# Kernel tuning notes

Measured on AMD Instinct MI355X. Metric: run time of the kernel, lower is better.

## Reference

```python
import jax, jax.numpy as jnp
import numpy as np

MD = 20          # max_displacement
TEMP = 1e-4      # softmax temperature
B, C, H, W = 4, 64, 112, 112


def setup_inputs() -> dict:
    key = jax.random.key(0)
    k1, k2 = jax.random.split(key)
    in1 = jax.random.normal(k1, (B, C, H, W), dtype=jnp.float32)
    in2 = jax.random.normal(k2, (B, C, H, W), dtype=jnp.float32)
    return {"in1": in1, "in2": in2}


def reference(in1, in2):
    b, c, h, w = in1.shape
    # F.normalize(x, dim=1): x / max(||x||_2, eps)
    def l2n(x):
        return x / jnp.maximum(jnp.linalg.norm(x, axis=1, keepdims=True), 1e-12)
    in1 = l2n(in1)
    in2 = l2n(in2)

    pad = jnp.pad(in2, ((0, 0), (0, 0), (MD, MD), (MD, MD)))

    d = jnp.arange(-MD, MD + 1)
    dx, dy = jnp.meshgrid(d, d, indexing="ij")  # torch.meshgrid default 'ij'
    dx = dx.reshape(-1)  # [K] with K = (2*MD+1)^2
    dy = dy.reshape(-1)

    def sim_one(dxi, dyi):
        # shifted window of padded in2, same spatial size as in1
        sl = jax.lax.dynamic_slice(pad, (0, 0, MD + dxi, MD + dyi), (b, c, h, w))
        return jnp.sum(in1 * sl, axis=1)  # [B,H,W]

    sim = jax.vmap(sim_one)(dx, dy)          # [K,B,H,W]
    sim = jnp.transpose(sim, (1, 0, 2, 3))   # [B,K,H,W] cost volume

    weights = jax.nn.softmax(sim / TEMP, axis=1)  # softmax over displacements
    guide = jnp.stack((dx, dy), axis=-1).astype(jnp.float32)  # [K,2]
    # flow[b,d,h,w] = sum_k weights[b,k,h,w] * guide[k,d]
    flow = jnp.einsum("bkhw,kd->bdhw", weights, guide)
    return flow
```

## Files before the change

kernel.cpp:

```cpp
#include <hip/hip_runtime.h>
#include <math.h>

#define BB 4
#define CC 64
#define HH 112
#define WW 112
#define MD 20
#define KD 41
#define SCALE 10000.0f
#define NPIX (BB*HH*WW)
#define NT 10
#define ROW2 (NT*2*2*64*8)
#define IN2S_BYTES ((size_t)BB*HH*ROW2*2)

typedef _Float16 half8   __attribute__((ext_vector_type(8)));
typedef float    f32x4   __attribute__((ext_vector_type(4)));
typedef unsigned short ushort8 __attribute__((ext_vector_type(8)));

static __device__ __forceinline__ unsigned short f2h_bits(float x) {
    _Float16 h = (_Float16)x;
    return __builtin_bit_cast(unsigned short, h);
}
static __device__ __forceinline__ float h2f(unsigned short s) {
    return (float)__builtin_bit_cast(_Float16, s);
}

__global__ __launch_bounds__(256) void prep_kernel(const float* __restrict__ in1,
                                                   const float* __restrict__ in2,
                                                   unsigned short* __restrict__ in2s,
                                                   float* __restrict__ inv1) {
    __shared__ float sinv2[WW];
    int bid = blockIdx.x;
    int b = bid / HH, h = bid % HH;
    int t = threadIdx.x;

    if (t < WW) {
        float s = 0.f;
        for (int c = 0; c < CC; ++c) {
            float x = in2[((b*CC + c)*HH + h)*WW + t];
            s += x*x;
        }
        sinv2[t] = 1.0f / fmaxf(sqrtf(s), 1e-12f);
    } else if (t >= 128 && t < 128 + WW) {
        int w = t - 128;
        float s = 0.f;
        for (int c = 0; c < CC; ++c) {
            float x = in1[((b*CC + c)*HH + h)*WW + w];
            s += x*x;
        }
        inv1[(b*HH + h)*WW + w] = 1.0f / fmaxf(sqrtf(s), 1e-12f);
    }
    __syncthreads();

    int wave = t >> 6, lane = t & 63;
    int n = lane & 15, q = lane >> 4;
    unsigned short* base = in2s + (size_t)(b*HH + h)*ROW2;
    for (int tsk = wave; tsk < NT*2; tsk += 4) {
        int tau = tsk >> 1, ks = tsk & 1;
        int p = 16*tau + n, col = p - MD;
        ushort8 hb = {0,0,0,0,0,0,0,0}, lb = {0,0,0,0,0,0,0,0};
        if (col >= 0 && col < WW) {
            float iv = sinv2[col];
            #pragma unroll
            for (int j = 0; j < 8; ++j) {
                int c = 32*ks + 8*q + j;
                float x = in2[((b*CC + c)*HH + h)*WW + col] * iv;
                unsigned short xh = f2h_bits(x);
                float r = (x - h2f(xh)) * 4096.0f;
                hb[j] = xh;
                lb[j] = f2h_bits(r);
            }
        }
        *(ushort8*)(base + (size_t)((tau*4 + ks*2 + 0)*64 + lane)*8) = hb;
        *(ushort8*)(base + (size_t)((tau*4 + ks*2 + 1)*64 + lane)*8) = lb;
    }
}

__global__ __launch_bounds__(64, 3) void corr_kernel(const float* __restrict__ in1,
                                                     const unsigned short* __restrict__ in2s,
                                                     const float* __restrict__ inv1,
                                                     float* __restrict__ out) {
    int gid = blockIdx.x;
    int wt  = gid / (BB*HH);
    int rem = gid % (BB*HH);
    int b = rem / HH, h = rem % HH;
    int lane = threadIdx.x;
    int n = lane & 15, q = lane >> 4;
    int m0 = 4*q;

    int wA = wt*16 + n;
    float i1 = inv1[(b*HH + h)*WW + wA];
    half8 aH[2], aL[2];
    #pragma unroll
    for (int ks = 0; ks < 2; ++ks) {
        #pragma unroll
        for (int j = 0; j < 8; ++j) {
            int c = 32*ks + 8*q + j;
            float x = in1[((b*CC + c)*HH + h)*WW + wA] * i1;
            _Float16 xh = (_Float16)x;
            aH[ks][j] = xh;
            aL[ks][j] = (_Float16)((x - (float)xh) * 4096.0f);
        }
    }

    float nm20[4]; bool v0[4], v2[4], v3[4];
    #pragma unroll
    for (int r = 0; r < 4; ++r) {
        int nm = n - (m0 + r);
        nm20[r] = (float)(nm - 20);
        v0[r] = (nm >= 0);
        v2[r] = (nm <= 8);
        v3[r] = (nm <= -8);
    }

    float sm[4], sl[4], ssx[4], ssy[4];
    #pragma unroll
    for (int r = 0; r < 4; ++r) { sm[r] = -3.0f; sl[r] = 0.f; ssx[r] = 0.f; ssy[r] = 0.f; }

    int dlo = max(0, MD - h);
    int dhi = min(KD, HH + MD - h);

    for (int dxi = dlo; dxi < dhi; ++dxi) {
        const unsigned short* rb = in2s + (size_t)(b*HH + (h + dxi - MD))*ROW2;
        f32x4 s[4];
        #pragma unroll
        for (int oi = 0; oi < 4; ++oi) {
            int tau = wt + oi;
            const half8* fp = (const half8*)(rb + (size_t)(tau*4*64 + lane)*8);
            half8 bH0 = fp[0];
            half8 bL0 = fp[64];
            half8 bH1 = fp[128];
            half8 bL1 = fp[192];
            f32x4 a0 = {0.f,0.f,0.f,0.f}, a1 = {0.f,0.f,0.f,0.f};
            a0 = __builtin_amdgcn_mfma_f32_16x16x32_f16(aH[0], bH0, a0, 0, 0, 0);
            a1 = __builtin_amdgcn_mfma_f32_16x16x32_f16(aH[0], bL0, a1, 0, 0, 0);
            a1 = __builtin_amdgcn_mfma_f32_16x16x32_f16(aL[0], bH0, a1, 0, 0, 0);
            a0 = __builtin_amdgcn_mfma_f32_16x16x32_f16(aH[1], bH1, a0, 0, 0, 0);
            a1 = __builtin_amdgcn_mfma_f32_16x16x32_f16(aH[1], bL1, a1, 0, 0, 0);
            a1 = __builtin_amdgcn_mfma_f32_16x16x32_f16(aL[1], bH1, a1, 0, 0, 0);
            s[oi] = a0 + a1 * (1.0f/4096.0f);
        }
        float dxf = (float)(dxi - MD);
        #pragma unroll
        for (int r = 0; r < 4; ++r) {
            float s0v = v0[r] ? s[0][r] : -3.0f;
            float s1v = s[1][r];
            float s2v = v2[r] ? s[2][r] : -3.0f;
            float s3v = v3[r] ? s[3][r] : -3.0f;
            float mn = fmaxf(fmaxf(sm[r], s0v), fmaxf(fmaxf(s1v, s2v), s3v));
            float er = __expf((sm[r] - mn)*SCALE);
            float e0 = __expf((s0v - mn)*SCALE);
            float e1 = __expf((s1v - mn)*SCALE);
            float e2 = __expf((s2v - mn)*SCALE);
            float e3 = __expf((s3v - mn)*SCALE);
            float sum = (e0 + e1) + (e2 + e3);
            float tt  = e1 + 2.f*e2 + 3.f*e3;
            sl[r]  = sl[r]*er + sum;
            ssx[r] = ssx[r]*er + dxf*sum;
            ssy[r] = ssy[r]*er + (16.f*tt + nm20[r]*sum);
            sm[r]  = mn;
        }
    }

    int nlo = dlo, nhi = KD - dhi;
    if (nlo + nhi > 0) {
        float sdx = 0.f;
        for (int d = 0; d < nlo; ++d)  sdx += (float)(d - MD);
        for (int d = dhi; d < KD; ++d) sdx += (float)(d - MD);
        float cnt = (float)((nlo + nhi)*KD);
        #pragma unroll
        for (int r = 0; r < 4; ++r) {
            float mn = fmaxf(sm[r], 0.f);
            float er = __expf((sm[r] - mn)*SCALE);
            float e0 = __expf((0.f - mn)*SCALE);
            sl[r]  = sl[r]*er + cnt*e0;
            ssx[r] = ssx[r]*er + (float)KD*sdx*e0;
            ssy[r] = ssy[r]*er;
            sm[r]  = mn;
        }
    }

    #pragma unroll
    for (int off = 1; off < 16; off <<= 1) {
        #pragma unroll
        for (int r = 0; r < 4; ++r) {
            float m2 = __shfl_xor(sm[r],  off);
            float l2 = __shfl_xor(sl[r],  off);
            float x2 = __shfl_xor(ssx[r], off);
            float y2 = __shfl_xor(ssy[r], off);
            float mn = fmaxf(sm[r], m2);
            float ea = __expf((sm[r] - mn)*SCALE);
            float eb = __expf((m2    - mn)*SCALE);
            sl[r]  = sl[r]*ea  + l2*eb;
            ssx[r] = ssx[r]*ea + x2*eb;
            ssy[r] = ssy[r]*ea + y2*eb;
            sm[r]  = mn;
        }
    }

    if (n == 0) {
        #pragma unroll
        for (int r = 0; r < 4; ++r) {
            int w = wt*16 + m0 + r;
            out[((b*2 + 0)*HH + h)*WW + w] = ssx[r] / sl[r];
            out[((b*2 + 1)*HH + h)*WW + w] = ssy[r] / sl[r];
        }
    }
}

extern "C" void kernel_launch(void* const* d_in, const int* in_sizes, int n_in,
                              void* d_out, int out_size, void* d_ws, size_t ws_size,
                              hipStream_t stream) {
    const float* in1 = (const float*)d_in[0];
    const float* in2 = (const float*)d_in[1];
    float* out = (float*)d_out;
    unsigned short* in2s = (unsigned short*)d_ws;
    float* inv1 = (float*)((char*)d_ws + IN2S_BYTES);

    prep_kernel<<<BB*HH, 256, 0, stream>>>(in1, in2, in2s, inv1);
    corr_kernel<<<7*BB*HH, 64, 0, stream>>>(in1, in2s, inv1, out);
}
```

Baseline: 187.9 us.

## Stage in2 tile in LDS, fuse in1 norm into corr, remap blocks per XCD

The pack kernel now loads each in2 row into a shared-memory tile once and reuses it for both the norm and the split-fp16 packing. It no longer computes the in1 norms; the correlation kernel computes them itself with cross-lane shuffles. The correlation kernel uses 128-thread blocks holding two rows 56 apart, and maps block ids so each XCD works on one batch and half the rows, aiming to improve L2 locality of in2s. It also switches to exp2 with a prescaled constant, loads all B fragments before the MFMAs, and drops the occupancy hint from the launch bounds.

```diff
diff --git a/kernel.cpp b/kernel.cpp
--- a/kernel.cpp
+++ b/kernel.cpp
@@ -1,5 +1,4 @@
 #include <hip/hip_runtime.h>
-#include <math.h>
 
 #define BB 4
 #define CC 64
@@ -7,16 +6,15 @@
 #define WW 112
 #define MD 20
 #define KD 41
-#define SCALE 10000.0f
-#define NPIX (BB*HH*WW)
+#define S2 14426.950408f
 #define NT 10
 #define ROW2 (NT*2*2*64*8)
-#define IN2S_BYTES ((size_t)BB*HH*ROW2*2)
 
 typedef _Float16 half8   __attribute__((ext_vector_type(8)));
 typedef float    f32x4   __attribute__((ext_vector_type(4)));
 typedef unsigned short ushort8 __attribute__((ext_vector_type(8)));
 
+static __device__ __forceinline__ float fmax_f(float a, float b) { return a > b ? a : b; }
 static __device__ __forceinline__ unsigned short f2h_bits(float x) {
     _Float16 h = (_Float16)x;
     return __builtin_bit_cast(unsigned short, h);
@@ -24,51 +22,59 @@
 static __device__ __forceinline__ float h2f(unsigned short s) {
     return (float)__builtin_bit_cast(_Float16, s);
 }
-
-__global__ __launch_bounds__(256) void prep_kernel(const float* __restrict__ in1,
-                                                   const float* __restrict__ in2,
-                                                   unsigned short* __restrict__ in2s,
-                                                   float* __restrict__ inv1) {
-    __shared__ float sinv2[WW];
-    int bid = blockIdx.x;
-    int b = bid / HH, h = bid % HH;
+static __device__ __forceinline__ f32x4 vmax4(f32x4 a, f32x4 b) {
+    f32x4 r;
+    #pragma unroll
+    for (int k = 0; k < 4; ++k) r[k] = a[k] > b[k] ? a[k] : b[k];
+    return r;
+}
+static __device__ __forceinline__ f32x4 vexp4(f32x4 d) {
+    f32x4 r;
+    #pragma unroll
+    for (int k = 0; k < 4; ++k) r[k] = __builtin_amdgcn_exp2f(d[k]);
+    return r;
+}
+static __device__ __forceinline__ f32x4 mfma16(half8 a, half8 b, f32x4 c) {
+    return __builtin_amdgcn_mfma_f32_16x16x32_f16(a, b, c, 0, 0, 0);
+}
+
+__global__ __launch_bounds__(256) void pack_kernel(const float* __restrict__ in2,
+                                                   unsigned short* __restrict__ in2s) {
+    __shared__ float tile[CC][WW + 1];
+    __shared__ float sinv[WW];
+    int b = blockIdx.x / HH, h = blockIdx.x % HH;
     int t = threadIdx.x;
-
+    const float* src = in2 + ((size_t)(b*CC)*HH + h)*WW;
+
+    for (int i = t; i < CC*WW; i += 256) {
+        int c = i / WW, w = i % WW;
+        tile[c][w] = src[(size_t)c*(HH*WW) + w];
+    }
+    __syncthreads();
     if (t < WW) {
         float s = 0.f;
-        for (int c = 0; c < CC; ++c) {
-            float x = in2[((b*CC + c)*HH + h)*WW + t];
-            s += x*x;
-        }
-        sinv2[t] = 1.0f / fmaxf(sqrtf(s), 1e-12f);
-    } else if (t >= 128 && t < 128 + WW) {
-        int w = t - 128;
-        float s = 0.f;
-        for (int c = 0; c < CC; ++c) {
-            float x = in1[((b*CC + c)*HH + h)*WW + w];
-            s += x*x;
-        }
-        inv1[(b*HH + h)*WW + w] = 1.0f / fmaxf(sqrtf(s), 1e-12f);
+        #pragma unroll
+        for (int c = 0; c < CC; ++c) { float x = tile[c][t]; s += x*x; }
+        sinv[t] = 1.0f / fmax_f(__builtin_sqrtf(s), 1e-12f);
     }
     __syncthreads();
 
-    int wave = t >> 6, lane = t & 63;
+    int wv = t >> 6, lane = t & 63;
     int n = lane & 15, q = lane >> 4;
     unsigned short* base = in2s + (size_t)(b*HH + h)*ROW2;
-    for (int tsk = wave; tsk < NT*2; tsk += 4) {
-        int tau = tsk >> 1, ks = tsk & 1;
-        int p = 16*tau + n, col = p - MD;
+    for (int u = wv; u < NT*2; u += 4) {
+        int tau = u >> 1, ks = u & 1;
+        int col = 16*tau + n - MD;
         ushort8 hb = {0,0,0,0,0,0,0,0}, lb = {0,0,0,0,0,0,0,0};
         if (col >= 0 && col < WW) {
-            float iv = sinv2[col];
+            float iv = sinv[col];
             #pragma unroll
             for (int j = 0; j < 8; ++j) {
                 int c = 32*ks + 8*q + j;
-                float x = in2[((b*CC + c)*HH + h)*WW + col] * iv;
+                float x = tile[c][col] * iv;
                 unsigned short xh = f2h_bits(x);
-                float r = (x - h2f(xh)) * 4096.0f;
                 hb[j] = xh;
-                lb[j] = f2h_bits(r);
+                lb[j] = f2h_bits((x - h2f(xh)) * 4096.0f);
             }
         }
         *(ushort8*)(base + (size_t)((tau*4 + ks*2 + 0)*64 + lane)*8) = hb;
@@ -76,134 +82,149 @@
     }
 }
 
-__global__ __launch_bounds__(64, 3) void corr_kernel(const float* __restrict__ in1,
-                                                     const unsigned short* __restrict__ in2s,
-                                                     const float* __restrict__ inv1,
-                                                     float* __restrict__ out) {
+__global__ __launch_bounds__(128) void corr_kernel(const float* __restrict__ in1,
+                                                   const unsigned short* __restrict__ in2s,
+                                                   float* __restrict__ out) {
     int gid = blockIdx.x;
-    int wt  = gid / (BB*HH);
-    int rem = gid % (BB*HH);
-    int b = rem / HH, h = rem % HH;
-    int lane = threadIdx.x;
+    int xcd = gid & 7;
+    int s   = gid >> 3;
+    int b   = xcd >> 1;
+    int p   = (xcd & 1)*28 + (s % 28);
+    int wt  = s / 28;
+    int wv  = threadIdx.x >> 6;
+    int h   = p + 56*wv;
+    int lane = threadIdx.x & 63;
     int n = lane & 15, q = lane >> 4;
     int m0 = 4*q;
-
     int wA = wt*16 + n;
-    float i1 = inv1[(b*HH + h)*WW + wA];
+
+    const float* a_src = in1 + ((size_t)(b*CC)*HH + h)*WW + wA;
+    float x[16];
+    float ss = 0.f;
+    #pragma unroll
+    for (int ks = 0; ks < 2; ++ks)
+        #pragma unroll
+        for (int j = 0; j < 8; ++j) {
+            float v = a_src[(size_t)(32*ks + 8*q + j)*(HH*WW)];
+            x[ks*8 + j] = v;
+            ss += v*v;
+        }
+    ss += __shfl_xor(ss, 16);
+    ss += __shfl_xor(ss, 32);
+    float i1 = 1.0f / fmax_f(__builtin_sqrtf(ss), 1e-12f);
     half8 aH[2], aL[2];
     #pragma unroll
-    for (int ks = 0; ks < 2; ++ks) {
+    for (int ks = 0; ks < 2; ++ks)
         #pragma unroll
         for (int j = 0; j < 8; ++j) {
-            int c = 32*ks + 8*q + j;
-            float x = in1[((b*CC + c)*HH + h)*WW + wA] * i1;
-            _Float16 xh = (_Float16)x;
-            aH[ks][j] = xh;
-            aL[ks][j] = (_Float16)((x - (float)xh) * 4096.0f);
-        }
-    }
-
-    float nm20[4]; bool v0[4], v2[4], v3[4];
+            float v = x[ks*8 + j] * i1;
+            _Float16 vh = (_Float16)v;
+            aH[ks][j] = vh;
+            aL[ks][j] = (_Float16)((v - (float)vh) * 4096.0f);
+        }
+
+    f32x4 NM20; bool v0b[4], v2b[4], v3b[4];
     #pragma unroll
     for (int r = 0; r < 4; ++r) {
         int nm = n - (m0 + r);
-        nm20[r] = (float)(nm - 20);
-        v0[r] = (nm >= 0);
-        v2[r] = (nm <= 8);
-        v3[r] = (nm <= -8);
-    }
-
-    float sm[4], sl[4], ssx[4], ssy[4];
-    #pragma unroll
-    for (int r = 0; r < 4; ++r) { sm[r] = -3.0f; sl[r] = 0.f; ssx[r] = 0.f; ssy[r] = 0.f; }
-
-    int dlo = max(0, MD - h);
-    int dhi = min(KD, HH + MD - h);
+        NM20[r] = (float)(nm - 20);
+        v0b[r] = (nm >= 0);
+        v2b[r] = (nm <= 8);
+        v3b[r] = (nm <= -8);
+    }
+
+    f32x4 SM = {-4.f,-4.f,-4.f,-4.f}, SL = {0.f,0.f,0.f,0.f};
+    f32x4 SSX = {0.f,0.f,0.f,0.f}, SSY = {0.f,0.f,0.f,0.f};
+
+    int dlo = MD - h > 0 ? MD - h : 0;
+    int dhi = (HH + MD - h) < KD ? (HH + MD - h) : KD;
 
     for (int dxi = dlo; dxi < dhi; ++dxi) {
         const unsigned short* rb = in2s + (size_t)(b*HH + (h + dxi - MD))*ROW2;
-        f32x4 s[4];
+        half8 bf[4][4];
         #pragma unroll
         for (int oi = 0; oi < 4; ++oi) {
-            int tau = wt + oi;
-            const half8* fp = (const half8*)(rb + (size_t)(tau*4*64 + lane)*8);
-            half8 bH0 = fp[0];
-            half8 bL0 = fp[64];
-            half8 bH1 = fp[128];
-            half8 bL1 = fp[192];
+            const half8* fp = (const half8*)(rb + (size_t)((wt + oi)*4*64 + lane)*8);
+            bf[oi][0] = fp[0];
+            bf[oi][1] = fp[64];
+            bf[oi][2] = fp[128];
+            bf[oi][3] = fp[192];
+        }
+        f32x4 sv[4];
+        #pragma unroll
+        for (int oi = 0; oi < 4; ++oi) {
             f32x4 a0 = {0.f,0.f,0.f,0.f}, a1 = {0.f,0.f,0.f,0.f};
-            a0 = __builtin_amdgcn_mfma_f32_16x16x32_f16(aH[0], bH0, a0, 0, 0, 0);
-            a1 = __builtin_amdgcn_mfma_f32_16x16x32_f16(aH[0], bL0, a1, 0, 0, 0);
-            a1 = __builtin_amdgcn_mfma_f32_16x16x32_f16(aL[0], bH0, a1, 0, 0, 0);
-            a0 = __builtin_amdgcn_mfma_f32_16x16x32_f16(aH[1], bH1, a0, 0, 0, 0);
-            a1 = __builtin_amdgcn_mfma_f32_16x16x32_f16(aH[1], bL1, a1, 0, 0, 0);
-            a1 = __builtin_amdgcn_mfma_f32_16x16x32_f16(aL[1], bH1, a1, 0, 0, 0);
-            s[oi] = a0 + a1 * (1.0f/4096.0f);
-        }
+            a0 = mfma16(aH[0], bf[oi][0], a0);
+            a1 = mfma16(aH[0], bf[oi][1], a1);
+            a1 = mfma16(aL[0], bf[oi][0], a1);
+            a0 = mfma16(aH[1], bf[oi][2], a0);
+            a1 = mfma16(aH[1], bf[oi][3], a1);
+            a1 = mfma16(aL[1], bf[oi][2], a1);
+            sv[oi] = a0 + a1 * (1.0f/4096.0f);
+        }
+        f32x4 V0, V1 = sv[1], V2, V3;
+        #pragma unroll
+        for (int r = 0; r < 4; ++r) {
+            V0[r] = v0b[r] ? sv[0][r] : -4.0f;
+            V2[r] = v2b[r] ? sv[2][r] : -4.0f;
+            V3[r] = v3b[r] ? sv[3][r] : -4.0f;
+        }
+        f32x4 MN = vmax4(vmax4(SM, V0), vmax4(V1, vmax4(V2, V3)));
+        f32x4 ER = vexp4((SM - MN) * S2);
+        f32x4 E0 = vexp4((V0 - MN) * S2);
+        f32x4 E1 = vexp4((V1 - MN) * S2);
+        f32x4 E2 = vexp4((V2 - MN) * S2);
+        f32x4 E3 = vexp4((V3 - MN) * S2);
+        f32x4 SUM = (E0 + E1) + (E2 + E3);
+        f32x4 TT  = E1 + E2*2.0f + E3*3.0f;
         float dxf = (float)(dxi - MD);
-        #pragma unroll
-        for (int r = 0; r < 4; ++r) {
-            float s0v = v0[r] ? s[0][r] : -3.0f;
-            float s1v = s[1][r];
-            float s2v = v2[r] ? s[2][r] : -3.0f;
-            float s3v = v3[r] ? s[3][r] : -3.0f;
-            float mn = fmaxf(fmaxf(sm[r], s0v), fmaxf(fmaxf(s1v, s2v), s3v));
-            float er = __expf((sm[r] - mn)*SCALE);
-            float e0 = __expf((s0v - mn)*SCALE);
-            float e1 = __expf((s1v - mn)*SCALE);
-            float e2 = __expf((s2v - mn)*SCALE);
-            float e3 = __expf((s3v - mn)*SCALE);
-            float sum = (e0 + e1) + (e2 + e3);
-            float tt  = e1 + 2.f*e2 + 3.f*e3;
-            sl[r]  = sl[r]*er + sum;
-            ssx[r] = ssx[r]*er + dxf*sum;
-            ssy[r] = ssy[r]*er + (16.f*tt + nm20[r]*sum);
-            sm[r]  = mn;
-        }
-    }
-
-    int nlo = dlo, nhi = KD - dhi;
-    if (nlo + nhi > 0) {
+        SL  = SL *ER + SUM;
+        SSX = SSX*ER + SUM*dxf;
+        SSY = SSY*ER + (TT*16.0f + NM20*SUM);
+        SM  = MN;
+    }
+
+    int miss = dlo + (KD - dhi);
+    if (miss > 0) {
         float sdx = 0.f;
-        for (int d = 0; d < nlo; ++d)  sdx += (float)(d - MD);
+        for (int d = 0; d < dlo; ++d)  sdx += (float)(d - MD);
         for (int d = dhi; d < KD; ++d) sdx += (float)(d - MD);
-        float cnt = (float)((nlo + nhi)*KD);
-        #pragma unroll
-        for (int r = 0; r < 4; ++r) {
-            float mn = fmaxf(sm[r], 0.f);
-            float er = __expf((sm[r] - mn)*SCALE);
-            float e0 = __expf((0.f - mn)*SCALE);
-            sl[r]  = sl[r]*er + cnt*e0;
-            ssx[r] = ssx[r]*er + (float)KD*sdx*e0;
-            ssy[r] = ssy[r]*er;
-            sm[r]  = mn;
-        }
+        float cnt = (float)miss * (float)KD;
+        f32x4 Z = {0.f,0.f,0.f,0.f};
+        f32x4 MN = vmax4(SM, Z);
+        f32x4 ER = vexp4((SM - MN) * S2);
+        f32x4 E0 = vexp4((Z  - MN) * S2);
+        SL  = SL *ER + E0*cnt;
+        SSX = SSX*ER + E0*((float)KD*sdx);
+        SSY = SSY*ER;
+        SM  = MN;
     }
 
     #pragma unroll
     for (int off = 1; off < 16; off <<= 1) {
-        #pragma unroll
-        for (int r = 0; r < 4; ++r) {
-            float m2 = __shfl_xor(sm[r],  off);
-            float l2 = __shfl_xor(sl[r],  off);
-            float x2 = __shfl_xor(ssx[r], off);
-            float y2 = __shfl_xor(ssy[r], off);
-            float mn = fmaxf(sm[r], m2);
-            float ea = __expf((sm[r] - mn)*SCALE);
-            float eb = __expf((m2    - mn)*SCALE);
-            sl[r]  = sl[r]*ea  + l2*eb;
-            ssx[r] = ssx[r]*ea + x2*eb;
-            ssy[r] = ssy[r]*ea + y2*eb;
-            sm[r]  = mn;
-        }
+        f32x4 M2, L2, X2, Y2;
+        #pragma unroll
+        for (int k = 0; k < 4; ++k) {
+            M2[k] = __shfl_xor(SM[k],  off);
+            L2[k] = __shfl_xor(SL[k],  off);
+            X2[k] = __shfl_xor(SSX[k], off);
+            Y2[k] = __shfl_xor(SSY[k], off);
+        }
+        f32x4 MN = vmax4(SM, M2);
+        f32x4 EA = vexp4((SM - MN) * S2);
+        f32x4 EB = vexp4((M2 - MN) * S2);
+        SL  = SL *EA + L2*EB;
+        SSX = SSX*EA + X2*EB;
+        SSY = SSY*EA + Y2*EB;
+        SM  = MN;
     }
 
     if (n == 0) {
         #pragma unroll
         for (int r = 0; r < 4; ++r) {
             int w = wt*16 + m0 + r;
-            out[((b*2 + 0)*HH + h)*WW + w] = ssx[r] / sl[r];
-            out[((b*2 + 1)*HH + h)*WW + w] = ssy[r] / sl[r];
+            out[((b*2 + 0)*HH + h)*WW + w] = SSX[r] / SL[r];
+            out[((b*2 + 1)*HH + h)*WW + w] = SSY[r] / SL[r];
         }
     }
 }
@@ -215,8 +236,7 @@
     const float* in2 = (const float*)d_in[1];
     float* out = (float*)d_out;
     unsigned short* in2s = (unsigned short*)d_ws;
-    float* inv1 = (float*)((char*)d_ws + IN2S_BYTES);
-
-    prep_kernel<<<BB*HH, 256, 0, stream>>>(in1, in2, in2s, inv1);
-    corr_kernel<<<7*BB*HH, 64, 0, stream>>>(in1, in2s, inv1, out);
-}
+
+    pack_kernel<<<BB*HH, 256, 0, stream>>>(in2, in2s);
+    corr_kernel<<<8*196, 128, 0, stream>>>(in1, in2s, out);
+}
```

After: 165.2 us. 12.1% less time.
